# Kernel optimization log

Measured on AMD Instinct MI355X. Metric: run time of the kernel, lower is better.

Reference implementation:

```python
import jax, jax.numpy as jnp
import numpy as np

N_NODES, D, H, L, E, N_DST = 100000, 64, 8, 3, 100000, 50000
HD = H * D
LEAKY_ALPHA = 0.01


def setup_inputs() -> dict:
    key = jax.random.key(0)
    ks = jax.random.split(key, 8)
    features = jax.random.normal(ks[0], (N_NODES, D), dtype=jnp.float32)
    edge_metapath_indices = jax.random.randint(ks[1], (E, L), 0, N_NODES)
    dst = jax.random.randint(ks[2], (E,), 0, N_DST)
    s = 1.0 / np.sqrt(HD)
    W_ih = jax.random.uniform(ks[3], (3 * HD, D), jnp.float32, -s, s)
    W_hh = jax.random.uniform(ks[4], (3 * HD, HD), jnp.float32, -s, s)
    b_ih = jax.random.uniform(ks[5], (3 * HD,), jnp.float32, -s, s)
    b_hh = jax.random.uniform(ks[6], (3 * HD,), jnp.float32, -s, s)
    attn = jax.random.normal(ks[7], (1, H, D), dtype=jnp.float32) * (1.414 / np.sqrt(D))
    return {"features": features, "W_ih": W_ih, "W_hh": W_hh, "b_ih": b_ih,
            "b_hh": b_hh, "attn": attn,
            "edge_metapath_indices": edge_metapath_indices, "dst": dst,
            "num_dst": N_DST}


def _gru_last_hidden(x_seq, W_ih, W_hh, b_ih, b_hh):
    # x_seq: [L, E, D]; torch nn.GRU gate math, return final hidden [E, HD]
    h0 = jnp.zeros((x_seq.shape[1], HD), dtype=x_seq.dtype)

    def step(h, x):
        gi = x @ W_ih.T + b_ih            # [E, 3HD]
        gh = h @ W_hh.T + b_hh            # [E, 3HD]
        i_r, i_z, i_n = jnp.split(gi, 3, axis=-1)
        h_r, h_z, h_n = jnp.split(gh, 3, axis=-1)
        r = jax.nn.sigmoid(i_r + h_r)
        z = jax.nn.sigmoid(i_z + h_z)
        n = jnp.tanh(i_n + r * h_n)
        h_new = (1.0 - z) * n + z * h
        return h_new, None

    h_last, _ = jax.lax.scan(step, h0, x_seq)
    return h_last


def reference(features, W_ih, W_hh, b_ih, b_hh, attn,
              edge_metapath_indices, dst, num_dst):
    # gather metapath node embeddings: [E, L, D]
    edata = features[edge_metapath_indices]
    # per-edge GRU over the metapath sequence -> final hidden [E, HD]
    hidden = _gru_last_hidden(jnp.transpose(edata, (1, 0, 2)), W_ih, W_hh, b_ih, b_hh)
    eft = hidden.reshape(-1, H, D)                         # [E, H, D]
    # attention logits per edge/head + leaky relu
    a = jnp.sum(eft * attn, axis=-1)                       # [E, H]
    a = jnp.where(a > 0, a, LEAKY_ALPHA * a)
    # edge softmax over destination-node segments (stable)
    a_max = jax.ops.segment_max(a, dst, num_segments=num_dst)    # [ND, H]
    a_exp = jnp.exp(a - a_max[dst])
    a_sum = jax.ops.segment_sum(a_exp, dst, num_segments=num_dst)
    alpha = a_exp / a_sum[dst]                             # [E, H]
    # scatter-sum aggregation of attention-weighted edge features
    ft = jax.ops.segment_sum(eft * alpha[:, :, None], dst, num_segments=num_dst)
    return ft                                              # [ND, H, D]
```

## Files before the change

kernel.cpp:

```cpp
#include <hip/hip_runtime.h>

typedef __attribute__((ext_vector_type(8))) short bf16x8;
typedef __attribute__((ext_vector_type(4))) float f32x4;

#define E_N   100000
#define ND_N  50000
#define NN_N  100000
#define SLOTS 32

__device__ __forceinline__ float b2f(unsigned short u) {
    return __uint_as_float(((unsigned int)u) << 16);
}
__device__ __forceinline__ unsigned short f2b(float f) {
    unsigned int b = __float_as_uint(f);
    b += 0x7fffu + ((b >> 16) & 1u);
    return (unsigned short)(b >> 16);
}
__device__ __forceinline__ float frcp(float x) { return __builtin_amdgcn_rcpf(x); }
__device__ __forceinline__ float fsig(float x) { return frcp(1.f + __expf(-x)); }
__device__ __forceinline__ float ftanhf(float x) {
    float e = __expf(2.f * x);
    return 1.f - 2.f * frcp(e + 1.f);
}

#define GLDS16(g, l)                                                        \
    __builtin_amdgcn_global_load_lds(                                       \
        (const __attribute__((address_space(1))) void*)(g),                 \
        (__attribute__((address_space(3))) void*)(l), 16, 0, 0)

__global__ void conv_f2b(const float* __restrict__ src, unsigned short* __restrict__ dst, int n4) {
    int i = blockIdx.x * 256 + threadIdx.x;
    if (i < n4) {
        float4 v = ((const float4*)src)[i];
        ushort4 o;
        o.x = f2b(v.x); o.y = f2b(v.y); o.z = f2b(v.z); o.w = f2b(v.w);
        ((ushort4*)dst)[i] = o;
    }
}

__global__ void zero_u4(uint4* __restrict__ p, int n4) {
    int i = blockIdx.x * 256 + threadIdx.x;
    if (i < n4) p[i] = make_uint4(0u, 0u, 0u, 0u);
}

template<int G2>
__device__ __forceinline__ void mma_tile(
    const unsigned char* __restrict__ lds_a, const unsigned char* __restrict__ lds_b,
    f32x4 acc[4][2][2], int wm, int wn, int l15, int hi8)
{
    #pragma unroll
    for (int kk = 0; kk < 2; ++kk) {
        const int kb = kk * 64 + hi8 * 2;
        bf16x8 a[2];
        #pragma unroll
        for (int mi = 0; mi < 2; ++mi) {
            int row = wm * 32 + mi * 16 + l15;
            a[mi] = *(const bf16x8*)(lds_a + row * 128 + (kb ^ ((row & 7) << 4)));
        }
        #pragma unroll
        for (int g = 0; g < 3; ++g) {
            const int gi = (g == 2) ? G2 : g;
            bf16x8 b[2];
            #pragma unroll
            for (int ni = 0; ni < 2; ++ni) {
                int brow = g * 64 + wn * 32 + ni * 16 + l15;
                b[ni] = *(const bf16x8*)(lds_b + brow * 128 + (kb ^ ((brow & 7) << 4)));
            }
            #pragma unroll
            for (int mi = 0; mi < 2; ++mi)
                #pragma unroll
                for (int ni = 0; ni < 2; ++ni)
                    acc[gi][mi][ni] = __builtin_amdgcn_mfma_f32_16x16x32_bf16(
                        a[mi], b[ni], acc[gi][mi][ni], 0, 0, 0);
        }
    }
}

__global__ __launch_bounds__(512, 4) void gru_step(
    const unsigned short* __restrict__ feat16,
    const int* __restrict__ emi,
    const unsigned short* __restrict__ hprev,
    unsigned short* __restrict__ hnext,
    const unsigned short* __restrict__ wih,
    const unsigned short* __restrict__ whh,
    const float* __restrict__ bih,
    const float* __restrict__ bhh,
    int t)
{
    __shared__ __align__(16) unsigned char lds_a[128 * 128];
    __shared__ __align__(16) unsigned char lds_b[192 * 128];

    const int tid = threadIdx.x;
    const int nwg = gridDim.x;
    const int logical = (blockIdx.x & 7) * (nwg >> 3) + (blockIdx.x >> 3);
    const int mb = (logical >> 3) * 128;
    const int nb = (logical & 7) * 64;

    const int lane = tid & 63;
    const int wid  = tid >> 6;
    const int wm   = wid >> 1;
    const int wn   = wid & 1;
    const int l15  = lane & 15;
    const int hi8  = (lane >> 4) * 8;

    f32x4 acc[4][2][2];
    #pragma unroll
    for (int g = 0; g < 4; ++g)
        #pragma unroll
        for (int mi = 0; mi < 2; ++mi)
            #pragma unroll
            for (int ni = 0; ni < 2; ++ni) {
                f32x4 zz = {0.f, 0.f, 0.f, 0.f};
                acc[g][mi][ni] = zz;
            }

    int a_row[2], a_sl2[2], a_er[2];
    #pragma unroll
    for (int q = 0; q < 2; ++q) {
        int c = tid + q * 512;
        a_row[q] = c >> 3;
        a_sl2[q] = (c & 7) ^ (a_row[q] & 7);
        int er = mb + a_row[q];
        a_er[q] = er < E_N ? er : E_N - 1;
    }
    int b_wr[3], b_sl2[3];
    #pragma unroll
    for (int q = 0; q < 3; ++q) {
        int c = tid + q * 512;
        int row = c >> 3;
        b_sl2[q] = (c & 7) ^ (row & 7);
        b_wr[q]  = (row >> 6) * 512 + nb + (row & 63);
    }

    #pragma unroll
    for (int q = 0; q < 2; ++q) {
        int node = emi[a_er[q] * 3 + t];
        GLDS16(feat16 + (size_t)node * 64 + a_sl2[q] * 8, lds_a + (tid + q * 512) * 16);
    }
    #pragma unroll
    for (int q = 0; q < 3; ++q)
        GLDS16(wih + (size_t)b_wr[q] * 64 + b_sl2[q] * 8, lds_b + (tid + q * 512) * 16);
    __syncthreads();
    mma_tile<2>(lds_a, lds_b, acc, wm, wn, l15, hi8);
    __syncthreads();

    if (t > 0) {
        const unsigned short* asrc[2];
        const unsigned short* bsrc[3];
        #pragma unroll
        for (int q = 0; q < 2; ++q) asrc[q] = hprev + (size_t)a_er[q] * 512 + a_sl2[q] * 8;
        #pragma unroll
        for (int q = 0; q < 3; ++q) bsrc[q] = whh + (size_t)b_wr[q] * 512 + b_sl2[q] * 8;

        for (int kt = 0; kt < 8; ++kt) {
            const int k0 = kt * 64;
            #pragma unroll
            for (int q = 0; q < 2; ++q)
                GLDS16(asrc[q] + k0, lds_a + (tid + q * 512) * 16);
            #pragma unroll
            for (int q = 0; q < 3; ++q)
                GLDS16(bsrc[q] + k0, lds_b + (tid + q * 512) * 16);
            __syncthreads();
            mma_tile<3>(lds_a, lds_b, acc, wm, wn, l15, hi8);
            __syncthreads();
        }
    }

    #pragma unroll
    for (int ni = 0; ni < 2; ++ni) {
        const int col = nb + wn * 32 + ni * 16 + l15;
        const float br0  = bih[col] + bhh[col];
        const float bz0  = bih[512 + col] + bhh[512 + col];
        const float bin_ = bih[1024 + col];
        const float bhn_ = bhh[1024 + col];
        #pragma unroll
        for (int mi = 0; mi < 2; ++mi) {
            const int rbase = mb + wm * 32 + mi * 16 + (lane >> 4) * 4;
            #pragma unroll
            for (int j = 0; j < 4; ++j) {
                const int row = rbase + j;
                if (row < E_N) {
                    float r = fsig(acc[0][mi][ni][j] + br0);
                    float z = fsig(acc[1][mi][ni][j] + bz0);
                    float n = ftanhf(acc[2][mi][ni][j] + bin_ + r * (acc[3][mi][ni][j] + bhn_));
                    float hold = (t > 0) ? b2f(hprev[(size_t)row * 512 + col]) : 0.f;
                    float hv = (1.f - z) * n + z * hold;
                    hnext[(size_t)row * 512 + col] = f2b(hv);
                }
            }
        }
    }
}

__global__ __launch_bounds__(256) void attn_logits(
    const unsigned short* __restrict__ hl, const float* __restrict__ attnw,
    float* __restrict__ a)
{
    int e = blockIdx.x * 4 + (threadIdx.x >> 6);
    int lane = threadIdx.x & 63;
    uint4 v = *(const uint4*)(hl + (size_t)e * 512 + lane * 8);
    int h = lane >> 3;
    int dp = (lane & 7) * 8;
    float4 w0 = *(const float4*)(attnw + h * 64 + dp);
    float4 w1 = *(const float4*)(attnw + h * 64 + dp + 4);
    const unsigned short* u = (const unsigned short*)&v;
    float s = b2f(u[0]) * w0.x + b2f(u[1]) * w0.y + b2f(u[2]) * w0.z + b2f(u[3]) * w0.w
            + b2f(u[4]) * w1.x + b2f(u[5]) * w1.y + b2f(u[6]) * w1.z + b2f(u[7]) * w1.w;
    s += __shfl_xor(s, 1);
    s += __shfl_xor(s, 2);
    s += __shfl_xor(s, 4);
    if ((lane & 7) == 0)
        a[e * 8 + h] = s > 0.f ? s : 0.01f * s;
}

__global__ __launch_bounds__(256) void build_lists(
    const int* __restrict__ dstp, int* __restrict__ cnt, int* __restrict__ lists)
{
    int e = blockIdx.x * 256 + threadIdx.x;
    if (e < E_N) {
        int d = dstp[e];
        int slot = atomicAdd(&cnt[d], 1);
        if (slot < SLOTS) lists[(size_t)d * SLOTS + slot] = e;
    }
}

__global__ __launch_bounds__(256) void aggregate(
    const unsigned short* __restrict__ hl, const float* __restrict__ a,
    const int* __restrict__ lists, const int* __restrict__ cnt,
    float* __restrict__ out)
{
    int d = blockIdx.x * 4 + (threadIdx.x >> 6);
    int lane = threadIdx.x & 63;
    int n = cnt[d];
    n = n < SLOTS ? n : SLOTS;
    const int h = lane >> 3;
    const int* lst = lists + (size_t)d * SLOTS;

    float m = -1e30f;
    for (int i = 0; i < n; ++i)
        m = fmaxf(m, a[lst[i] * 8 + h]);
    float s = 0.f;
    for (int i = 0; i < n; ++i)
        s += __expf(a[lst[i] * 8 + h] - m);
    float rs = frcp(s);

    float acc[8] = {0.f, 0.f, 0.f, 0.f, 0.f, 0.f, 0.f, 0.f};
    for (int i = 0; i < n; ++i) {
        int e = lst[i];
        float alpha = __expf(a[e * 8 + h] - m) * rs;
        uint4 v = *(const uint4*)(hl + (size_t)e * 512 + lane * 8);
        const unsigned short* u = (const unsigned short*)&v;
        #pragma unroll
        for (int j = 0; j < 8; ++j)
            acc[j] += alpha * b2f(u[j]);
    }
    float4 o0 = {acc[0], acc[1], acc[2], acc[3]};
    float4 o1 = {acc[4], acc[5], acc[6], acc[7]};
    float* op = out + (size_t)d * 512 + lane * 8;
    *(float4*)op = o0;
    *(float4*)(op + 4) = o1;
}

extern "C" void kernel_launch(void* const* d_in, const int* in_sizes, int n_in,
                              void* d_out, int out_size, void* d_ws, size_t ws_size,
                              hipStream_t stream)
{
    const float* features = (const float*)d_in[0];
    const float* W_ih     = (const float*)d_in[1];
    const float* W_hh     = (const float*)d_in[2];
    const float* b_ih     = (const float*)d_in[3];
    const float* b_hh     = (const float*)d_in[4];
    const float* attnw    = (const float*)d_in[5];
    const int*   emi      = (const int*)d_in[6];
    const int*   dstp     = (const int*)d_in[7];

    char* ws = (char*)d_ws;
    size_t off = 0;
    auto alloc = [&](size_t bytes) -> void* {
        void* p = ws + off;
        off = (off + bytes + 255) & ~(size_t)255;
        return p;
    };
    unsigned short* feat16 = (unsigned short*)alloc((size_t)NN_N * 64 * 2);
    unsigned short* wih16  = (unsigned short*)alloc((size_t)1536 * 64 * 2);
    unsigned short* whh16  = (unsigned short*)alloc((size_t)1536 * 512 * 2);
    unsigned short* h0     = (unsigned short*)alloc((size_t)E_N * 512 * 2);
    unsigned short* h1     = (unsigned short*)alloc((size_t)E_N * 512 * 2);
    float*          abuf   = (float*)alloc((size_t)E_N * 8 * 4);
    int*            cnt    = (int*)alloc((size_t)ND_N * 4);
    int*            lists  = (int*)alloc((size_t)ND_N * SLOTS * 4);

    conv_f2b<<<(NN_N * 64 / 4 + 255) / 256, 256, 0, stream>>>(features, feat16, NN_N * 64 / 4);
    conv_f2b<<<(1536 * 64 / 4 + 255) / 256, 256, 0, stream>>>(W_ih, wih16, 1536 * 64 / 4);
    conv_f2b<<<(1536 * 512 / 4 + 255) / 256, 256, 0, stream>>>(W_hh, whh16, 1536 * 512 / 4);

    zero_u4<<<(ND_N / 4 + 255) / 256, 256, 0, stream>>>((uint4*)cnt, ND_N / 4);

    const int grid = ((E_N + 127) / 128) * 8;
    gru_step<<<grid, 512, 0, stream>>>(feat16, emi, nullptr, h0, wih16, whh16, b_ih, b_hh, 0);
    gru_step<<<grid, 512, 0, stream>>>(feat16, emi, h0, h1, wih16, whh16, b_ih, b_hh, 1);
    gru_step<<<grid, 512, 0, stream>>>(feat16, emi, h1, h0, wih16, whh16, b_ih, b_hh, 2);

    attn_logits<<<E_N / 4, 256, 0, stream>>>(h0, attnw, abuf);
    build_lists<<<(E_N + 255) / 256, 256, 0, stream>>>(dstp, cnt, lists);
    aggregate<<<ND_N / 4, 256, 0, stream>>>(h0, abuf, lists, cnt, (float*)d_out);
}
```

Measured before the change: 809.3 us.

## Double-buffer GRU recurrent K-loop, reuse hprev tile, stage output through LDS

Moves the gru_step recurrent GEMM to two 40 KB LDS buffers so the next K-slice of hprev/W_hh loads while MFMAs run on the current one. The input-projection tile and the first recurrent tile are issued together behind one wait-plus-barrier. The previous hidden values needed for the gate blend are read from the already-staged LDS tile instead of a second scattered global read. Outputs are written to LDS and then stored as coalesced 16-byte rows. LDS use rises to 80 KB per block, which may cut occupancy below the launch_bounds target of 4 blocks.

```diff
diff --git a/kernel.cpp b/kernel.cpp
--- a/kernel.cpp
+++ b/kernel.cpp
@@ -27,6 +27,18 @@
     __builtin_amdgcn_global_load_lds(                                       \
         (const __attribute__((address_space(1))) void*)(g),                 \
         (__attribute__((address_space(3))) void*)(l), 16, 0, 0)
+
+__device__ __forceinline__ void wait_and_barrier() {
+    __builtin_amdgcn_sched_barrier(0);
+    asm volatile("s_waitcnt vmcnt(0)" ::: "memory");
+    __builtin_amdgcn_s_barrier();
+    __builtin_amdgcn_sched_barrier(0);
+}
+__device__ __forceinline__ void plain_barrier() {
+    __builtin_amdgcn_sched_barrier(0);
+    __builtin_amdgcn_s_barrier();
+    __builtin_amdgcn_sched_barrier(0);
+}
 
 __global__ void conv_f2b(const float* __restrict__ src, unsigned short* __restrict__ dst, int n4) {
     int i = blockIdx.x * 256 + threadIdx.x;
@@ -45,9 +57,11 @@
 
 template<int G2>
 __device__ __forceinline__ void mma_tile(
-    const unsigned char* __restrict__ lds_a, const unsigned char* __restrict__ lds_b,
+    const unsigned char* __restrict__ buf,
     f32x4 acc[4][2][2], int wm, int wn, int l15, int hi8)
 {
+    const unsigned char* lds_a = buf;
+    const unsigned char* lds_b = buf + 16384;
     #pragma unroll
     for (int kk = 0; kk < 2; ++kk) {
         const int kb = kk * 64 + hi8 * 2;
@@ -87,14 +101,14 @@
     const float* __restrict__ bhh,
     int t)
 {
-    __shared__ __align__(16) unsigned char lds_a[128 * 128];
-    __shared__ __align__(16) unsigned char lds_b[192 * 128];
+    __shared__ __align__(16) unsigned char lds_mem[2 * 40960];
 
     const int tid = threadIdx.x;
     const int nwg = gridDim.x;
     const int logical = (blockIdx.x & 7) * (nwg >> 3) + (blockIdx.x >> 3);
     const int mb = (logical >> 3) * 128;
     const int nb = (logical & 7) * 64;
+    const int hold_kt = nb >> 6;
 
     const int lane = tid & 63;
     const int wid  = tid >> 6;
@@ -114,13 +128,13 @@
                 acc[g][mi][ni] = zz;
             }
 
-    int a_row[2], a_sl2[2], a_er[2];
+    int a_sl2[2], a_er[2];
     #pragma unroll
     for (int q = 0; q < 2; ++q) {
         int c = tid + q * 512;
-        a_row[q] = c >> 3;
-        a_sl2[q] = (c & 7) ^ (a_row[q] & 7);
-        int er = mb + a_row[q];
+        int row = c >> 3;
+        a_sl2[q] = (c & 7) ^ (row & 7);
+        int er = mb + row;
         a_er[q] = er < E_N ? er : E_N - 1;
     }
     int b_wr[3], b_sl2[3];
@@ -135,37 +149,66 @@
     #pragma unroll
     for (int q = 0; q < 2; ++q) {
         int node = emi[a_er[q] * 3 + t];
-        GLDS16(feat16 + (size_t)node * 64 + a_sl2[q] * 8, lds_a + (tid + q * 512) * 16);
+        GLDS16(feat16 + (size_t)node * 64 + a_sl2[q] * 8, lds_mem + (tid + q * 512) * 16);
     }
     #pragma unroll
     for (int q = 0; q < 3; ++q)
-        GLDS16(wih + (size_t)b_wr[q] * 64 + b_sl2[q] * 8, lds_b + (tid + q * 512) * 16);
-    __syncthreads();
-    mma_tile<2>(lds_a, lds_b, acc, wm, wn, l15, hi8);
-    __syncthreads();
-
+        GLDS16(wih + (size_t)b_wr[q] * 64 + b_sl2[q] * 8,
+               lds_mem + 16384 + (tid + q * 512) * 16);
     if (t > 0) {
-        const unsigned short* asrc[2];
-        const unsigned short* bsrc[3];
-        #pragma unroll
-        for (int q = 0; q < 2; ++q) asrc[q] = hprev + (size_t)a_er[q] * 512 + a_sl2[q] * 8;
-        #pragma unroll
-        for (int q = 0; q < 3; ++q) bsrc[q] = whh + (size_t)b_wr[q] * 512 + b_sl2[q] * 8;
-
+        #pragma unroll
+        for (int q = 0; q < 2; ++q)
+            GLDS16(hprev + (size_t)a_er[q] * 512 + a_sl2[q] * 8,
+                   lds_mem + 40960 + (tid + q * 512) * 16);
+        #pragma unroll
+        for (int q = 0; q < 3; ++q)
+            GLDS16(whh + (size_t)b_wr[q] * 512 + b_sl2[q] * 8,
+                   lds_mem + 40960 + 16384 + (tid + q * 512) * 16);
+    }
+    wait_and_barrier();
+
+    mma_tile<2>(lds_mem, acc, wm, wn, l15, hi8);
+    plain_barrier();
+
+    unsigned int holdp[2][2][2] = {{{0u,0u},{0u,0u}},{{0u,0u},{0u,0u}}};
+
+    if (t > 0) {
+        #pragma unroll
         for (int kt = 0; kt < 8; ++kt) {
-            const int k0 = kt * 64;
-            #pragma unroll
-            for (int q = 0; q < 2; ++q)
-                GLDS16(asrc[q] + k0, lds_a + (tid + q * 512) * 16);
-            #pragma unroll
-            for (int q = 0; q < 3; ++q)
-                GLDS16(bsrc[q] + k0, lds_b + (tid + q * 512) * 16);
-            __syncthreads();
-            mma_tile<3>(lds_a, lds_b, acc, wm, wn, l15, hi8);
-            __syncthreads();
-        }
-    }
-
+            unsigned char*       wr = lds_mem + (kt & 1) * 40960;
+            const unsigned char* rd = lds_mem + ((kt & 1) ^ 1) * 40960;
+            if (kt < 7) {
+                const int k1 = (kt + 1) * 64;
+                #pragma unroll
+                for (int q = 0; q < 2; ++q)
+                    GLDS16(hprev + (size_t)a_er[q] * 512 + k1 + a_sl2[q] * 8,
+                           wr + (tid + q * 512) * 16);
+                #pragma unroll
+                for (int q = 0; q < 3; ++q)
+                    GLDS16(whh + (size_t)b_wr[q] * 512 + k1 + b_sl2[q] * 8,
+                           wr + 16384 + (tid + q * 512) * 16);
+            }
+            if (kt == hold_kt) {
+                #pragma unroll
+                for (int ni = 0; ni < 2; ++ni)
+                    #pragma unroll
+                    for (int mi = 0; mi < 2; ++mi)
+                        #pragma unroll
+                        for (int jp = 0; jp < 2; ++jp) {
+                            int r0 = wm * 32 + mi * 16 + (lane >> 4) * 4 + jp * 2;
+                            int r1 = r0 + 1;
+                            int ac = (wn * 32 + ni * 16 + l15) * 2;
+                            unsigned int lo = *(const unsigned short*)(rd + r0 * 128 + (ac ^ ((r0 & 7) << 4)));
+                            unsigned int hi = *(const unsigned short*)(rd + r1 * 128 + (ac ^ ((r1 & 7) << 4)));
+                            holdp[ni][mi][jp] = lo | (hi << 16);
+                        }
+            }
+            mma_tile<3>(rd, acc, wm, wn, l15, hi8);
+            wait_and_barrier();
+        }
+    }
+
+    unsigned char* lout = lds_mem;
     #pragma unroll
     for (int ni = 0; ni < 2; ++ni) {
         const int col = nb + wn * 32 + ni * 16 + l15;
@@ -175,19 +218,30 @@
         const float bhn_ = bhh[1024 + col];
         #pragma unroll
         for (int mi = 0; mi < 2; ++mi) {
-            const int rbase = mb + wm * 32 + mi * 16 + (lane >> 4) * 4;
             #pragma unroll
             for (int j = 0; j < 4; ++j) {
-                const int row = rbase + j;
-                if (row < E_N) {
-                    float r = fsig(acc[0][mi][ni][j] + br0);
-                    float z = fsig(acc[1][mi][ni][j] + bz0);
-                    float n = ftanhf(acc[2][mi][ni][j] + bin_ + r * (acc[3][mi][ni][j] + bhn_));
-                    float hold = (t > 0) ? b2f(hprev[(size_t)row * 512 + col]) : 0.f;
-                    float hv = (1.f - z) * n + z * hold;
-                    hnext[(size_t)row * 512 + col] = f2b(hv);
-                }
-            }
+                float r = fsig(acc[0][mi][ni][j] + br0);
+                float z = fsig(acc[1][mi][ni][j] + bz0);
+                float n = ftanhf(acc[2][mi][ni][j] + bin_ + r * (acc[3][mi][ni][j] + bhn_));
+                float hold = (t > 0)
+                    ? b2f((unsigned short)((holdp[ni][mi][j >> 1] >> ((j & 1) * 16)) & 0xffffu))
+                    : 0.f;
+                float hv = (1.f - z) * n + z * hold;
+                int row = wm * 32 + mi * 16 + (lane >> 4) * 4 + j;
+                int oc  = (wn * 32 + ni * 16 + l15) * 2;
+                *(unsigned short*)(lout + row * 128 + (oc ^ ((row & 7) << 4))) = f2b(hv);
+            }
+        }
+    }
+    __syncthreads();
+    #pragma unroll
+    for (int q = 0; q < 2; ++q) {
+        int chunk = tid + q * 512;
+        int row = chunk >> 3, c8 = chunk & 7;
+        int grow = mb + row;
+        if (grow < E_N) {
+            uint4 v = *(const uint4*)(lout + row * 128 + ((c8 * 16) ^ ((row & 7) << 4)));
+            *(uint4*)(hnext + (size_t)grow * 512 + nb + c8 * 8) = v;
         }
     }
 }
```

Result: faster. 740.8 us (-8.5%).
